# Performance work log

Hardware: AMD Instinct MI355X
Metric: run time of the kernel (lower is better)

## Reference

```python
import jax, jax.numpy as jnp
import numpy as np

N_NODES = 100000
N_EDGES = 1600000
EMB_DIM = 128
N_LAYERS = 3


def setup_inputs() -> dict:
    key = jax.random.key(0)
    k_emb, k_ws, k_wn, k_src, k_dst = jax.random.split(key, 5)
    scale = 1.0 / np.sqrt(EMB_DIM).astype(np.float32)
    emb_table = jax.random.normal(k_emb, (N_NODES, EMB_DIM), jnp.float32) * 0.02
    W_self = jax.random.normal(k_ws, (N_LAYERS, EMB_DIM, EMB_DIM), jnp.float32) * scale
    W_neigh = jax.random.normal(k_wn, (N_LAYERS, EMB_DIM, EMB_DIM), jnp.float32) * scale
    b = jnp.zeros((N_LAYERS, EMB_DIM), jnp.float32)
    src = jax.random.randint(k_src, (N_EDGES,), 0, N_NODES, jnp.int32)
    dst = jax.random.randint(k_dst, (N_EDGES,), 0, N_NODES, jnp.int32)
    return {"emb_table": emb_table, "W_self": W_self, "W_neigh": W_neigh,
            "b": b, "src": src, "dst": dst}


def reference(emb_table, W_self, W_neigh, b, src, dst):
    n = emb_table.shape[0]
    n_layers = W_self.shape[0]
    # in-degree per destination node, clamped to >=1 (DGL mean aggregator)
    deg = jax.ops.segment_sum(jnp.ones(src.shape[0], emb_table.dtype), dst, num_segments=n)
    inv_deg = (1.0 / jnp.maximum(deg, 1.0))[:, None]  # [N,1]
    x = emb_table
    for i in range(n_layers):
        # gather source features, mean-aggregate onto destinations
        neigh = jax.ops.segment_sum(x[src], dst, num_segments=n) * inv_deg  # [N,D]
        x = x @ W_self[i] + neigh @ W_neigh[i] + b[i]
        if i < n_layers - 1:
            x = jax.nn.relu(x)  # relu is idempotent: conv activation + outer relu
    return x
```

## Files before the change

kernel.cpp:

```cpp
#include <hip/hip_runtime.h>

#define EMB 128
#define CAP 64

typedef short bf16x8 __attribute__((ext_vector_type(8)));
typedef float f32x4 __attribute__((ext_vector_type(4)));

__device__ __forceinline__ float bf2f(unsigned int bits16) {
    return __uint_as_float(bits16 << 16);
}
__device__ __forceinline__ unsigned short f2bf(float f) {
    unsigned int u = __float_as_uint(f);
    u += 0x7FFF + ((u >> 16) & 1);
    return (unsigned short)(u >> 16);
}

__device__ __forceinline__ void place_edge(int ss, int dd, int lo, int hi,
                                           int* __restrict__ cnt, int* __restrict__ slot) {
    if (dd >= lo && dd < hi) {
        int pos = atomicAdd(&cnt[dd], 1);
        if (pos < CAP) slot[(size_t)dd * CAP + pos] = ss;
    }
}

__global__ void __launch_bounds__(256) scatter_pad_kernel(
        const int* __restrict__ src, const int* __restrict__ dst,
        int* __restrict__ cnt, int* __restrict__ slot, int e, int nr8, int n) {
    int r     = blockIdx.x & 7;
    int chunk = blockIdx.x >> 3;
    int lo = r * nr8;
    int hi = min(lo + nr8, n);
    int base = chunk * 1024 + (int)threadIdx.x * 4;
    if (base >= e) return;
    if (base + 4 <= e) {
        int4 s4 = *(const int4*)(src + base);
        int4 d4 = *(const int4*)(dst + base);
        place_edge(s4.x, d4.x, lo, hi, cnt, slot);
        place_edge(s4.y, d4.y, lo, hi, cnt, slot);
        place_edge(s4.z, d4.z, lo, hi, cnt, slot);
        place_edge(s4.w, d4.w, lo, hi, cnt, slot);
    } else {
        for (int i = base; i < e; ++i) place_edge(src[i], dst[i], lo, hi, cnt, slot);
    }
}

__global__ void cast_emb_kernel(const float* __restrict__ e,
                                unsigned short* __restrict__ xh, int total4) {
    int i = blockIdx.x * blockDim.x + threadIdx.x;
    if (i >= total4) return;
    float4 v = ((const float4*)e)[i];
    ushort4 o;
    o.x = f2bf(v.x); o.y = f2bf(v.y); o.z = f2bf(v.z); o.w = f2bf(v.w);
    ((ushort4*)xh)[i] = o;
}

__global__ void prep_w_kernel(const float* __restrict__ Ws, const float* __restrict__ Wn,
                              unsigned short* __restrict__ Wt, int total) {
    int i = blockIdx.x * blockDim.x + threadIdx.x;
    if (i >= total) return;
    int l   = i >> 15;
    int rem = i & 32767;
    int n   = rem >> 8;
    int kp  = rem & 255;
    int plane = kp >> 7;
    int kk    = kp & 127;
    const float* W = plane ? Wn : Ws;
    Wt[i] = f2bf(W[(size_t)l * EMB * EMB + kk * EMB + n]);
}

__global__ void __launch_bounds__(256) aggregate_bf_kernel(
        const unsigned short* __restrict__ xh, const int* __restrict__ cnt,
        const int* __restrict__ slot, unsigned short* __restrict__ nh, int n) {
    int node = blockIdx.x * 4 + (threadIdx.x >> 6);
    if (node >= n) return;
    int lane = threadIdx.x & 63;
    int craw = cnt[node];
    int m = min(craw, CAP);
    int myslot = (lane < m) ? slot[(size_t)node * CAP + lane] : 0;
    float ax = 0.f, ay = 0.f;
    int j = 0;
    for (; j + 8 <= m; j += 8) {
        int s0 = __shfl(myslot, j + 0), s1 = __shfl(myslot, j + 1);
        int s2 = __shfl(myslot, j + 2), s3 = __shfl(myslot, j + 3);
        int s4 = __shfl(myslot, j + 4), s5 = __shfl(myslot, j + 5);
        int s6 = __shfl(myslot, j + 6), s7 = __shfl(myslot, j + 7);
        unsigned int v0 = *(const unsigned int*)(xh + (size_t)s0 * EMB + lane * 2);
        unsigned int v1 = *(const unsigned int*)(xh + (size_t)s1 * EMB + lane * 2);
        unsigned int v2 = *(const unsigned int*)(xh + (size_t)s2 * EMB + lane * 2);
        unsigned int v3 = *(const unsigned int*)(xh + (size_t)s3 * EMB + lane * 2);
        unsigned int v4 = *(const unsigned int*)(xh + (size_t)s4 * EMB + lane * 2);
        unsigned int v5 = *(const unsigned int*)(xh + (size_t)s5 * EMB + lane * 2);
        unsigned int v6 = *(const unsigned int*)(xh + (size_t)s6 * EMB + lane * 2);
        unsigned int v7 = *(const unsigned int*)(xh + (size_t)s7 * EMB + lane * 2);
        ax += (bf2f(v0 & 0xFFFFu) + bf2f(v1 & 0xFFFFu)) + (bf2f(v2 & 0xFFFFu) + bf2f(v3 & 0xFFFFu))
            + (bf2f(v4 & 0xFFFFu) + bf2f(v5 & 0xFFFFu)) + (bf2f(v6 & 0xFFFFu) + bf2f(v7 & 0xFFFFu));
        ay += (bf2f(v0 >> 16) + bf2f(v1 >> 16)) + (bf2f(v2 >> 16) + bf2f(v3 >> 16))
            + (bf2f(v4 >> 16) + bf2f(v5 >> 16)) + (bf2f(v6 >> 16) + bf2f(v7 >> 16));
    }
    for (; j < m; ++j) {
        int s0 = __shfl(myslot, j);
        unsigned int v0 = *(const unsigned int*)(xh + (size_t)s0 * EMB + lane * 2);
        ax += bf2f(v0 & 0xFFFFu);
        ay += bf2f(v0 >> 16);
    }
    float sc = 1.0f / fmaxf((float)craw, 1.0f);
    unsigned int o = (unsigned int)f2bf(ax * sc) | ((unsigned int)f2bf(ay * sc) << 16);
    *(unsigned int*)(nh + (size_t)node * EMB + lane * 2) = o;
}

__global__ void __launch_bounds__(256) gemm_mfma_kernel(
        const unsigned short* __restrict__ xh, const unsigned short* __restrict__ nh,
        const unsigned short* __restrict__ Wt,
        const float* __restrict__ bias, float* __restrict__ outf,
        unsigned short* __restrict__ outh, int n, int do_relu) {
    __shared__ __align__(16) unsigned short a_s[128][32];
    __shared__ __align__(16) unsigned short b_s[128][32];

    int tid  = threadIdx.x;
    int w    = tid >> 6;
    int lane = tid & 63;
    int quad = lane >> 4;
    int l16  = lane & 15;
    int bm0  = blockIdx.x * 128;

    f32x4 acc[2][8];
    #pragma unroll
    for (int rt = 0; rt < 2; ++rt)
        #pragma unroll
        for (int ct = 0; ct < 8; ++ct)
            acc[rt][ct] = (f32x4){0.f, 0.f, 0.f, 0.f};

    for (int kc = 0; kc < 8; ++kc) {
        const unsigned short* Ap = (kc < 4) ? xh : nh;
        int kk0 = (kc & 3) * 32;
        #pragma unroll
        for (int h = 0; h < 2; ++h) {
            int c   = tid + h * 256;
            int row = c >> 2;
            int q   = (c & 3) * 8;
            int grr = bm0 + row; if (grr >= n) grr = n - 1;
            uint4 va = *(const uint4*)(Ap + (size_t)grr * EMB + kk0 + q);
            uint4 vb = *(const uint4*)(Wt + (size_t)row * 256 + kc * 32 + q);
            *(uint4*)&a_s[row][q] = va;
            *(uint4*)&b_s[row][q] = vb;
        }
        __syncthreads();
        bf16x8 af0 = *(const bf16x8*)&a_s[w * 32 + l16][quad * 8];
        bf16x8 af1 = *(const bf16x8*)&a_s[w * 32 + 16 + l16][quad * 8];
        #pragma unroll
        for (int ct = 0; ct < 8; ++ct) {
            bf16x8 bf = *(const bf16x8*)&b_s[ct * 16 + l16][quad * 8];
            acc[0][ct] = __builtin_amdgcn_mfma_f32_16x16x32_bf16(af0, bf, acc[0][ct], 0, 0, 0);
            acc[1][ct] = __builtin_amdgcn_mfma_f32_16x16x32_bf16(af1, bf, acc[1][ct], 0, 0, 0);
        }
        __syncthreads();
    }

    float bv[8];
    #pragma unroll
    for (int ct = 0; ct < 8; ++ct) bv[ct] = bias[ct * 16 + l16];
    #pragma unroll
    for (int rt = 0; rt < 2; ++rt) {
        #pragma unroll
        for (int r = 0; r < 4; ++r) {
            int grow = bm0 + w * 32 + rt * 16 + quad * 4 + r;
            if (grow >= n) continue;
            #pragma unroll
            for (int ct = 0; ct < 8; ++ct) {
                float v = acc[rt][ct][r] + bv[ct];
                if (do_relu) v = fmaxf(v, 0.f);
                int col = ct * 16 + l16;
                if (outf) outf[(size_t)grow * EMB + col] = v;
                else      outh[(size_t)grow * EMB + col] = f2bf(v);
            }
        }
    }
}

__global__ void hist_kernel(const int* __restrict__ dst, int* __restrict__ deg, int e) {
    int i = blockIdx.x * blockDim.x + threadIdx.x;
    int stride = gridDim.x * blockDim.x;
    for (; i < e; i += stride) atomicAdd(&deg[dst[i]], 1);
}

__global__ void __launch_bounds__(1024) scan_kernel(
        const int* __restrict__ deg, int* __restrict__ row_ptr,
        int* __restrict__ cursor, float* __restrict__ inv_deg, int n) {
    __shared__ int wave_tot[16];
    __shared__ int chunk_base_s;
    if (threadIdx.x == 0) chunk_base_s = 0;
    __syncthreads();
    int lane = threadIdx.x & 63;
    int wid  = threadIdx.x >> 6;
    for (int base = 0; base < n; base += 1024) {
        int i = base + (int)threadIdx.x;
        int v = (i < n) ? deg[i] : 0;
        int s = v;
        #pragma unroll
        for (int d = 1; d < 64; d <<= 1) {
            int t = __shfl_up(s, d, 64);
            if (lane >= d) s += t;
        }
        if (lane == 63) wave_tot[wid] = s;
        __syncthreads();
        int wsum = 0;
        for (int w2 = 0; w2 < wid; ++w2) wsum += wave_tot[w2];
        int excl = chunk_base_s + wsum + s - v;
        if (i < n) {
            row_ptr[i] = excl;
            cursor[i]  = excl;
            inv_deg[i] = 1.0f / fmaxf((float)v, 1.0f);
        }
        __syncthreads();
        if (threadIdx.x == 1023) chunk_base_s = excl + v;
        __syncthreads();
    }
    if (threadIdx.x == 0) row_ptr[n] = chunk_base_s;
}

__global__ void scatter_kernel(const int* __restrict__ src, const int* __restrict__ dst,
                               int* __restrict__ cursor, int* __restrict__ csr_src, int e) {
    int i = blockIdx.x * blockDim.x + threadIdx.x;
    if (i >= e) return;
    int d = dst[i];
    int pos = atomicAdd(&cursor[d], 1);
    csr_src[pos] = src[i];
}

__global__ void __launch_bounds__(256) aggregate_csr_kernel(
        const float* __restrict__ x, const int* __restrict__ row_ptr,
        const int* __restrict__ csr_src, const float* __restrict__ inv_deg,
        float* __restrict__ neigh, int n) {
    int node = blockIdx.x * 4 + (threadIdx.x >> 6);
    if (node >= n) return;
    int lane = threadIdx.x & 63;
    int beg = row_ptr[node];
    int end = row_ptr[node + 1];
    float ax = 0.f, ay = 0.f;
    for (int j = beg; j < end; ++j) {
        int s0 = csr_src[j];
        float2 v0 = *(const float2*)(x + (size_t)s0 * EMB + lane * 2);
        ax += v0.x;
        ay += v0.y;
    }
    float sc = inv_deg[node];
    *(float2*)(neigh + (size_t)node * EMB + lane * 2) = make_float2(ax * sc, ay * sc);
}

__global__ void __launch_bounds__(256) gemm_f32_kernel(
        const float* x, const float* __restrict__ neigh,
        const float* __restrict__ Ws, const float* __restrict__ Wn,
        const float* __restrict__ bias, float* out, int n, int do_relu) {
    __shared__ float s_ws[16][EMB];
    __shared__ float s_wn[16][EMB];
    __shared__ float s_x[16][68];
    __shared__ float s_n[16][68];
    int tid = threadIdx.x;
    int tc = tid & 31;
    int tr = tid >> 5;
    int bm0 = blockIdx.x * 64;
    float4 acc[8];
    #pragma unroll
    for (int r = 0; r < 8; ++r) acc[r] = make_float4(0.f, 0.f, 0.f, 0.f);
    for (int kc = 0; kc < 8; ++kc) {
        int k0 = kc * 16;
        const float4* wsv = (const float4*)(Ws + (size_t)k0 * EMB);
        const float4* wnv = (const float4*)(Wn + (size_t)k0 * EMB);
        ((float4*)s_ws)[tid] = wsv[tid];       ((float4*)s_ws)[tid + 256] = wsv[tid + 256];
        ((float4*)s_wn)[tid] = wnv[tid];       ((float4*)s_wn)[tid + 256] = wnv[tid + 256];
        int row = tid >> 2, kq = (tid & 3) * 4;
        int gr = bm0 + row;
        float4 vx = {0,0,0,0}, vn = {0,0,0,0};
        if (gr < n) {
            vx = *(const float4*)(x + (size_t)gr * EMB + k0 + kq);
            vn = *(const float4*)(neigh + (size_t)gr * EMB + k0 + kq);
        }
        s_x[kq+0][row] = vx.x; s_x[kq+1][row] = vx.y; s_x[kq+2][row] = vx.z; s_x[kq+3][row] = vx.w;
        s_n[kq+0][row] = vn.x; s_n[kq+1][row] = vn.y; s_n[kq+2][row] = vn.z; s_n[kq+3][row] = vn.w;
        __syncthreads();
        #pragma unroll
        for (int k = 0; k < 16; ++k) {
            float4 wa = *(const float4*)&s_ws[k][tc * 4];
            float4 wb = *(const float4*)&s_wn[k][tc * 4];
            float4 xv0 = *(const float4*)&s_x[k][tr * 8];
            float4 xv1 = *(const float4*)&s_x[k][tr * 8 + 4];
            float4 nv0 = *(const float4*)&s_n[k][tr * 8];
            float4 nv1 = *(const float4*)&s_n[k][tr * 8 + 4];
            #define ROWFMA(accv, xs, ns) \
                accv.x = fmaf(xs, wa.x, fmaf(ns, wb.x, accv.x)); \
                accv.y = fmaf(xs, wa.y, fmaf(ns, wb.y, accv.y)); \
                accv.z = fmaf(xs, wa.z, fmaf(ns, wb.z, accv.z)); \
                accv.w = fmaf(xs, wa.w, fmaf(ns, wb.w, accv.w));
            ROWFMA(acc[0], xv0.x, nv0.x) ROWFMA(acc[1], xv0.y, nv0.y)
            ROWFMA(acc[2], xv0.z, nv0.z) ROWFMA(acc[3], xv0.w, nv0.w)
            ROWFMA(acc[4], xv1.x, nv1.x) ROWFMA(acc[5], xv1.y, nv1.y)
            ROWFMA(acc[6], xv1.z, nv1.z) ROWFMA(acc[7], xv1.w, nv1.w)
            #undef ROWFMA
        }
        __syncthreads();
    }
    float4 bv = *(const float4*)(bias + tc * 4);
    #pragma unroll
    for (int r = 0; r < 8; ++r) {
        int gr = bm0 + tr * 8 + r;
        if (gr >= n) continue;
        float4 o = make_float4(acc[r].x + bv.x, acc[r].y + bv.y, acc[r].z + bv.z, acc[r].w + bv.w);
        if (do_relu) {
            o.x = fmaxf(o.x, 0.f); o.y = fmaxf(o.y, 0.f);
            o.z = fmaxf(o.z, 0.f); o.w = fmaxf(o.w, 0.f);
        }
        *(float4*)(out + (size_t)gr * EMB + tc * 4) = o;
    }
}

extern "C" void kernel_launch(void* const* d_in, const int* in_sizes, int n_in,
                              void* d_out, int out_size, void* d_ws, size_t ws_size,
                              hipStream_t stream) {
    const float* emb     = (const float*)d_in[0];
    const float* W_self  = (const float*)d_in[1];
    const float* W_neigh = (const float*)d_in[2];
    const float* bias    = (const float*)d_in[3];
    const int*   src     = (const int*)d_in[4];
    const int*   dst     = (const int*)d_in[5];
    const int N = in_sizes[0] / EMB;
    const int E = in_sizes[4];
    const int L = in_sizes[1] / (EMB * EMB);

    float* xout = (float*)d_out;

    auto align256 = [](size_t b) { return (b + 255) & ~(size_t)255; };
    size_t need_bf = align256((size_t)N * EMB * 2)
                   + align256((size_t)N * EMB * 2)
                   + align256((size_t)N * sizeof(int))
                   + align256((size_t)N * CAP * sizeof(int))
                   + align256((size_t)L * 32768 * 2);

    char* w = (char*)d_ws;
    auto alloc = [&](size_t bytes) {
        char* p = w;
        w += (bytes + 255) & ~(size_t)255;
        return p;
    };

    if (ws_size >= need_bf) {
        unsigned short* xh  = (unsigned short*)alloc((size_t)N * EMB * 2);
        unsigned short* nh  = (unsigned short*)alloc((size_t)N * EMB * 2);
        int*            cnt = (int*)alloc((size_t)N * sizeof(int));
        int*            slot= (int*)alloc((size_t)N * CAP * sizeof(int));
        unsigned short* Wt  = (unsigned short*)alloc((size_t)L * 32768 * 2);

        hipMemsetAsync(cnt, 0, (size_t)N * sizeof(int), stream);
        int nr8 = (N + 7) / 8;
        int chunks = (E + 1023) / 1024;
        scatter_pad_kernel<<<chunks * 8, 256, 0, stream>>>(src, dst, cnt, slot, E, nr8, N);
        cast_emb_kernel<<<(N * EMB / 4 + 255) / 256, 256, 0, stream>>>(emb, xh, N * EMB / 4);
        prep_w_kernel<<<(L * 32768 + 255) / 256, 256, 0, stream>>>(W_self, W_neigh, Wt, L * 32768);

        int gg = (N + 127) / 128;
        for (int l = 0; l < L; ++l) {
            aggregate_bf_kernel<<<(N + 3) / 4, 256, 0, stream>>>(xh, cnt, slot, nh, N);
            int last = (l == L - 1);
            gemm_mfma_kernel<<<gg, 256, 0, stream>>>(
                xh, nh, Wt + (size_t)l * 32768, bias + (size_t)l * EMB,
                last ? xout : nullptr, last ? nullptr : xh, N, last ? 0 : 1);
        }
    } else {
        float* neigh   = (float*)alloc((size_t)N * EMB * sizeof(float));
        int*   deg     = (int*)  alloc((size_t)N * sizeof(int));
        int*   row_ptr = (int*)  alloc((size_t)(N + 1) * sizeof(int));
        int*   cursor  = (int*)  alloc((size_t)N * sizeof(int));
        float* inv_deg = (float*)alloc((size_t)N * sizeof(float));
        int*   csr     = (int*)  alloc((size_t)E * sizeof(int));

        hipMemsetAsync(deg, 0, (size_t)N * sizeof(int), stream);
        hist_kernel<<<2048, 256, 0, stream>>>(dst, deg, E);
        scan_kernel<<<1, 1024, 0, stream>>>(deg, row_ptr, cursor, inv_deg, N);
        scatter_kernel<<<(E + 255) / 256, 256, 0, stream>>>(src, dst, cursor, csr, E);

        for (int l = 0; l < L; ++l) {
            const float* xin = (l == 0) ? emb : xout;
            aggregate_csr_kernel<<<(N + 3) / 4, 256, 0, stream>>>(xin, row_ptr, csr, inv_deg, neigh, N);
            gemm_f32_kernel<<<(N + 63) / 64, 256, 0, stream>>>(
                xin, neigh,
                W_self + (size_t)l * EMB * EMB, W_neigh + (size_t)l * EMB * EMB,
                bias + (size_t)l * EMB, xout, N, (l < L - 1) ? 1 : 0);
        }
    }
}
```

Measured before the change: 438.2 us.

## Split bf16 feature matrices into 8 column planes for cache-local gathers

```diff
diff --git a/kernel.cpp b/kernel.cpp
--- a/kernel.cpp
+++ b/kernel.cpp
@@ -44,14 +44,21 @@
     }
 }
 
-__global__ void cast_emb_kernel(const float* __restrict__ e,
-                                unsigned short* __restrict__ xh, int total4) {
-    int i = blockIdx.x * blockDim.x + threadIdx.x;
-    if (i >= total4) return;
-    float4 v = ((const float4*)e)[i];
-    ushort4 o;
-    o.x = f2bf(v.x); o.y = f2bf(v.y); o.z = f2bf(v.z); o.w = f2bf(v.w);
-    ((ushort4*)xh)[i] = o;
+__global__ void cast_emb_split_kernel(const float* __restrict__ e,
+                                      unsigned short* __restrict__ xh,
+                                      int n, int npl) {
+    int node = blockIdx.x * blockDim.x + threadIdx.x;
+    int p    = blockIdx.y;
+    if (node >= n) return;
+    const float4* s = (const float4*)(e + (size_t)node * EMB + p * 16);
+    float4 f0 = s[0], f1 = s[1], f2 = s[2], f3 = s[3];
+    ushort4 o0, o1, o2, o3;
+    o0.x = f2bf(f0.x); o0.y = f2bf(f0.y); o0.z = f2bf(f0.z); o0.w = f2bf(f0.w);
+    o1.x = f2bf(f1.x); o1.y = f2bf(f1.y); o1.z = f2bf(f1.z); o1.w = f2bf(f1.w);
+    o2.x = f2bf(f2.x); o2.y = f2bf(f2.y); o2.z = f2bf(f2.z); o2.w = f2bf(f2.w);
+    o3.x = f2bf(f3.x); o3.y = f2bf(f3.y); o3.z = f2bf(f3.z); o3.w = f2bf(f3.w);
+    ushort4* d = (ushort4*)(xh + (size_t)p * npl + (size_t)node * 16);
+    d[0] = o0; d[1] = o1; d[2] = o2; d[3] = o3;
 }
 
 __global__ void prep_w_kernel(const float* __restrict__ Ws, const float* __restrict__ Wn,
@@ -68,51 +75,53 @@
     Wt[i] = f2bf(W[(size_t)l * EMB * EMB + kk * EMB + n]);
 }
 
-__global__ void __launch_bounds__(256) aggregate_bf_kernel(
+__global__ void __launch_bounds__(256) aggregate_split_kernel(
         const unsigned short* __restrict__ xh, const int* __restrict__ cnt,
-        const int* __restrict__ slot, unsigned short* __restrict__ nh, int n) {
-    int node = blockIdx.x * 4 + (threadIdx.x >> 6);
-    if (node >= n) return;
-    int lane = threadIdx.x & 63;
-    int craw = cnt[node];
-    int m = min(craw, CAP);
-    int myslot = (lane < m) ? slot[(size_t)node * CAP + lane] : 0;
-    float ax = 0.f, ay = 0.f;
-    int j = 0;
-    for (; j + 8 <= m; j += 8) {
-        int s0 = __shfl(myslot, j + 0), s1 = __shfl(myslot, j + 1);
-        int s2 = __shfl(myslot, j + 2), s3 = __shfl(myslot, j + 3);
-        int s4 = __shfl(myslot, j + 4), s5 = __shfl(myslot, j + 5);
-        int s6 = __shfl(myslot, j + 6), s7 = __shfl(myslot, j + 7);
-        unsigned int v0 = *(const unsigned int*)(xh + (size_t)s0 * EMB + lane * 2);
-        unsigned int v1 = *(const unsigned int*)(xh + (size_t)s1 * EMB + lane * 2);
-        unsigned int v2 = *(const unsigned int*)(xh + (size_t)s2 * EMB + lane * 2);
-        unsigned int v3 = *(const unsigned int*)(xh + (size_t)s3 * EMB + lane * 2);
-        unsigned int v4 = *(const unsigned int*)(xh + (size_t)s4 * EMB + lane * 2);
-        unsigned int v5 = *(const unsigned int*)(xh + (size_t)s5 * EMB + lane * 2);
-        unsigned int v6 = *(const unsigned int*)(xh + (size_t)s6 * EMB + lane * 2);
-        unsigned int v7 = *(const unsigned int*)(xh + (size_t)s7 * EMB + lane * 2);
-        ax += (bf2f(v0 & 0xFFFFu) + bf2f(v1 & 0xFFFFu)) + (bf2f(v2 & 0xFFFFu) + bf2f(v3 & 0xFFFFu))
-            + (bf2f(v4 & 0xFFFFu) + bf2f(v5 & 0xFFFFu)) + (bf2f(v6 & 0xFFFFu) + bf2f(v7 & 0xFFFFu));
-        ay += (bf2f(v0 >> 16) + bf2f(v1 >> 16)) + (bf2f(v2 >> 16) + bf2f(v3 >> 16))
-            + (bf2f(v4 >> 16) + bf2f(v5 >> 16)) + (bf2f(v6 >> 16) + bf2f(v7 >> 16));
-    }
-    for (; j < m; ++j) {
-        int s0 = __shfl(myslot, j);
-        unsigned int v0 = *(const unsigned int*)(xh + (size_t)s0 * EMB + lane * 2);
-        ax += bf2f(v0 & 0xFFFFu);
-        ay += bf2f(v0 >> 16);
-    }
-    float sc = 1.0f / fmaxf((float)craw, 1.0f);
-    unsigned int o = (unsigned int)f2bf(ax * sc) | ((unsigned int)f2bf(ay * sc) << 16);
-    *(unsigned int*)(nh + (size_t)node * EMB + lane * 2) = o;
+        const int* __restrict__ slot, unsigned short* __restrict__ nh,
+        int n, int npl) {
+    int plane = blockIdx.x & 7;
+    int grp   = blockIdx.x >> 3;
+    int w     = threadIdx.x >> 6;
+    int lane  = threadIdx.x & 63;
+    int g     = lane >> 3;
+    int o     = lane & 7;
+    const unsigned short* xp = xh + (size_t)plane * npl;
+    unsigned short*       np = nh + (size_t)plane * npl;
+
+    #pragma unroll
+    for (int t = 0; t < 4; ++t) {
+        int node = grp * 16 + w * 4 + t;
+        if (node >= n) return;
+        int craw = __builtin_nontemporal_load(&cnt[node]);
+        int m = min(craw, CAP);
+        int myslot = 0;
+        if (lane < m) myslot = __builtin_nontemporal_load(&slot[(size_t)node * CAP + lane]);
+        float ax = 0.f, ay = 0.f;
+        for (int j = 0; j < m; j += 8) {
+            int e = j + g;
+            int s = __shfl(myslot, e);
+            if (e < m) {
+                unsigned int v = *(const unsigned int*)(xp + (size_t)s * 16 + o * 2);
+                ax += bf2f(v & 0xFFFFu);
+                ay += bf2f(v >> 16);
+            }
+        }
+        ax += __shfl_xor(ax, 8);  ay += __shfl_xor(ay, 8);
+        ax += __shfl_xor(ax, 16); ay += __shfl_xor(ay, 16);
+        ax += __shfl_xor(ax, 32); ay += __shfl_xor(ay, 32);
+        if (lane < 8) {
+            float sc = 1.0f / fmaxf((float)craw, 1.0f);
+            unsigned int ov = (unsigned int)f2bf(ax * sc) | ((unsigned int)f2bf(ay * sc) << 16);
+            *(unsigned int*)(np + (size_t)node * 16 + lane * 2) = ov;
+        }
+    }
 }
 
 __global__ void __launch_bounds__(256) gemm_mfma_kernel(
         const unsigned short* __restrict__ xh, const unsigned short* __restrict__ nh,
         const unsigned short* __restrict__ Wt,
         const float* __restrict__ bias, float* __restrict__ outf,
-        unsigned short* __restrict__ outh, int n, int do_relu) {
+        unsigned short* __restrict__ outh, int n, int npl, int do_relu) {
     __shared__ __align__(16) unsigned short a_s[128][32];
     __shared__ __align__(16) unsigned short b_s[128][32];
 
@@ -132,14 +141,16 @@
 
     for (int kc = 0; kc < 8; ++kc) {
         const unsigned short* Ap = (kc < 4) ? xh : nh;
-        int kk0 = (kc & 3) * 32;
         #pragma unroll
         for (int h = 0; h < 2; ++h) {
             int c   = tid + h * 256;
             int row = c >> 2;
             int q   = (c & 3) * 8;
             int grr = bm0 + row; if (grr >= n) grr = n - 1;
-            uint4 va = *(const uint4*)(Ap + (size_t)grr * EMB + kk0 + q);
+            int kk  = (kc & 3) * 32 + q;
+            int pl  = kk >> 4;
+            int off = kk & 15;
+            uint4 va = *(const uint4*)(Ap + (size_t)pl * npl + (size_t)grr * 16 + off);
             uint4 vb = *(const uint4*)(Wt + (size_t)row * 256 + kc * 32 + q);
             *(uint4*)&a_s[row][q] = va;
             *(uint4*)&b_s[row][q] = vb;
@@ -169,9 +180,8 @@
             for (int ct = 0; ct < 8; ++ct) {
                 float v = acc[rt][ct][r] + bv[ct];
                 if (do_relu) v = fmaxf(v, 0.f);
-                int col = ct * 16 + l16;
-                if (outf) outf[(size_t)grow * EMB + col] = v;
-                else      outh[(size_t)grow * EMB + col] = f2bf(v);
+                if (outf) outf[(size_t)grow * EMB + ct * 16 + l16] = v;
+                else      outh[(size_t)ct * npl + (size_t)grow * 16 + l16] = f2bf(v);
             }
         }
     }
@@ -325,6 +335,7 @@
     const int N = in_sizes[0] / EMB;
     const int E = in_sizes[4];
     const int L = in_sizes[1] / (EMB * EMB);
+    const int NPL = N * 16;
 
     float* xout = (float*)d_out;
 
@@ -353,16 +364,20 @@
         int nr8 = (N + 7) / 8;
         int chunks = (E + 1023) / 1024;
         scatter_pad_kernel<<<chunks * 8, 256, 0, stream>>>(src, dst, cnt, slot, E, nr8, N);
-        cast_emb_kernel<<<(N * EMB / 4 + 255) / 256, 256, 0, stream>>>(emb, xh, N * EMB / 4);
+        {
+            dim3 g((N + 255) / 256, 8);
+            cast_emb_split_kernel<<<g, 256, 0, stream>>>(emb, xh, N, NPL);
+        }
         prep_w_kernel<<<(L * 32768 + 255) / 256, 256, 0, stream>>>(W_self, W_neigh, Wt, L * 32768);
 
-        int gg = (N + 127) / 128;
+        int agg_grid  = ((N + 15) / 16) * 8;
+        int gemm_grid = (N + 127) / 128;
         for (int l = 0; l < L; ++l) {
-            aggregate_bf_kernel<<<(N + 3) / 4, 256, 0, stream>>>(xh, cnt, slot, nh, N);
+            aggregate_split_kernel<<<agg_grid, 256, 0, stream>>>(xh, cnt, slot, nh, N, NPL);
             int last = (l == L - 1);
-            gemm_mfma_kernel<<<gg, 256, 0, stream>>>(
+            gemm_mfma_kernel<<<gemm_grid, 256, 0, stream>>>(
                 xh, nh, Wt + (size_t)l * 32768, bias + (size_t)l * EMB,
-                last ? xout : nullptr, last ? nullptr : xh, N, last ? 0 : 1);
+                last ? xout : nullptr, last ? nullptr : xh, N, NPL, last ? 0 : 1);
         }
     } else {
         float* neigh   = (float*)alloc((size_t)N * EMB * sizeof(float));
```

Measured after the change: 980.2 us. 2.24x slower.
